# Kernel tuning notes

Measured on AMD Instinct MI355X. Metric: run time of the kernel, lower is better.

## Reference

```python
import jax, jax.numpy as jnp
import numpy as np
from itertools import permutations

NUM_LAYERS = 3
K = 5  # fixed node degree -> every Hungarian sub-problem is 5x5
# one-hot permutation tensor: P1H[p, r, c] = 1 iff permutation p assigns row r -> col c
PERMS = np.array(list(permutations(range(K))), dtype=np.int32)          # [120, K]
P1H = (PERMS[:, :, None] == np.arange(K)[None, None, :]).astype(np.float32)  # [120, K, K]


def _mlp(x, W1, b1, W2, b2):
    # 2-layer MLP with ReLU (repo's MLP(in, hid, out, 2))
    return jax.nn.relu(x @ W1 + b1) @ W2 + b2


def _sinkhorn(src, itera):
    s = jax.nn.softmax(src, axis=1)  # row-max subtraction is built in
    for i in range(itera):
        s = s / jnp.sum(s, axis=i % 2, keepdims=True)
    return jnp.nan_to_num(s)


def _masked_softmax(src):
    s1 = jnp.nan_to_num(jax.nn.softmax(src, axis=1))
    s2 = jnp.nan_to_num(jax.nn.softmax(src, axis=0))
    return (s1 + s2) * 0.5


def setup_inputs() -> dict:
    key = jax.random.key(0)
    ks = jax.random.split(key, 12)
    n1 = n2 = 1024
    hid = 64
    adj1 = jax.random.randint(ks[0], (n1, K), 0, n1)
    adj2 = jax.random.randint(ks[1], (n2, K), 0, n2)
    # adjacency matrices consistent with the neighbor lists
    G1 = jnp.zeros((n1, n1), jnp.float32).at[jnp.arange(n1)[:, None], adj1].set(1.0)
    G2 = jnp.zeros((n2, n2), jnp.float32).at[jnp.arange(n2)[:, None], adj2].set(1.0)
    s = 0.1
    return {
        'G1': G1, 'G2': G2, 'adj1': adj1, 'adj2': adj2,
        'ro_W1': jax.random.normal(ks[2], (NUM_LAYERS, 1, hid), jnp.float32) * s,
        'ro_b1': jax.random.normal(ks[3], (NUM_LAYERS, hid), jnp.float32) * s,
        'ro_W2': jax.random.normal(ks[4], (NUM_LAYERS, hid, 1), jnp.float32) * s,
        'ro_b2': jax.random.normal(ks[5], (NUM_LAYERS, 1), jnp.float32) * s,
        'fin_W1': jax.random.normal(ks[6], (1, hid), jnp.float32) * s,
        'fin_b1': jax.random.normal(ks[7], (hid,), jnp.float32) * s,
        'fin_W2': jax.random.normal(ks[8], (hid, 1), jnp.float32) * s,
        'fin_b2': jax.random.normal(ks[9], (1,), jnp.float32) * s,
    }


def reference(G1, G2, adj1, adj2, ro_W1, ro_b1, ro_W2, ro_b2, fin_W1, fin_b1, fin_W2, fin_b2):
    n1 = G1.shape[0]
    n2 = G2.shape[0]
    d1 = jnp.sum(G1, axis=1)
    d2 = jnp.sum(G2, axis=1)
    ttheta = jnp.mean(d1)
    # S[i, j, 0] = -|d1[i] - d2[j]|
    S = -jnp.abs(d1[:, None] - d2[None, :])[..., None]  # [n1, n2, 1]
    p1h = jnp.asarray(P1H)
    for li in range(NUM_LAYERS):
        Wn = _sinkhorn(_mlp(S / ttheta, ro_W1[li], ro_b1[li], ro_W2[li], ro_b2[li]).squeeze(-1), 5)
        W = jnp.log(Wn * (n1 * 1.5))
        W = jnp.where(jnp.isneginf(W), jnp.float32(-1e12), W)
        W = jnp.where(jnp.isposinf(W), jnp.float32(1e12), W)
        Wd = jax.lax.stop_gradient(W)  # matches W.detach().numpy()
        # small[a, b, r, c] = Wd[adj1[a, r], adj2[b, c]]  -> [n1, n2, K, K]
        small = jnp.transpose(Wd[adj1][:, :, adj2], (0, 2, 1, 3))
        # exact linear_sum_assignment(-small): maximize sum over the K! permutations
        scores = jnp.einsum('abrc,prc->abp', small, p1h)  # [n1, n2, 120]
        X1 = jnp.max(scores, axis=-1)                      # [n1, n2]
        S = X1[..., None]
    out = _masked_softmax(_mlp(S, fin_W1, fin_b1, fin_W2, fin_b2).squeeze(-1))
    return out
```

## Files before the change

### kernel.cpp

```cpp
#include <hip/hip_runtime.h>
#include <math.h>

#define N 1024
#define NB 256
#define KD 5
#define SL 8
#define MAGIC 0x13572468
#define FSTRIDE 32
#define FREGION (NB * FSTRIDE + FSTRIDE)


__device__ __forceinline__ float load_sc(const float* p){
  return __hip_atomic_load(p, __ATOMIC_RELAXED, __HIP_MEMORY_SCOPE_AGENT);
}
__device__ __forceinline__ void store_sc(float* p, float v){
  __hip_atomic_store(p, v, __ATOMIC_RELAXED, __HIP_MEMORY_SCOPE_AGENT);
}
__device__ __forceinline__ int load_sci(const int* p){
  return __hip_atomic_load(p, __ATOMIC_RELAXED, __HIP_MEMORY_SCOPE_AGENT);
}
__device__ __forceinline__ void store_sci(int* p, int v){
  __hip_atomic_store(p, v, __ATOMIC_RELAXED, __HIP_MEMORY_SCOPE_AGENT);
}

__device__ __forceinline__ void gbarS(int* flg){
  __builtin_amdgcn_s_waitcnt(0);
  __syncthreads();
  const int t = threadIdx.x, B = blockIdx.x;
  int* go = flg + NB * FSTRIDE;
  if (B == 0){
    if (t > 0 && t < NB){
      while (load_sci(&flg[t * FSTRIDE]) != MAGIC) __builtin_amdgcn_s_sleep(2);
    }
    __syncthreads();
    if (t == 0) store_sci(go, MAGIC);
  } else {
    if (t == 0){
      store_sci(&flg[B * FSTRIDE], MAGIC);
      while (load_sci(go) != MAGIC) __builtin_amdgcn_s_sleep(2);
    }
    __syncthreads();
  }
}

__device__ __forceinline__ float wred_sum(float v){
#pragma unroll
  for (int off = 32; off > 0; off >>= 1) v += __shfl_down(v, off);
  return v;
}
__device__ __forceinline__ void bsum4(float v[4], float* s64){
  float w0 = wred_sum(v[0]), w1 = wred_sum(v[1]), w2 = wred_sum(v[2]), w3 = wred_sum(v[3]);
  __syncthreads();
  int wv = threadIdx.x >> 6;
  if ((threadIdx.x & 63) == 0){ s64[wv*4] = w0; s64[wv*4+1] = w1; s64[wv*4+2] = w2; s64[wv*4+3] = w3; }
  __syncthreads();
  float r0 = 0.f, r1 = 0.f, r2 = 0.f, r3 = 0.f;
#pragma unroll
  for (int i = 0; i < 16; ++i){ r0 += s64[i*4]; r1 += s64[i*4+1]; r2 += s64[i*4+2]; r3 += s64[i*4+3]; }
  v[0] = r0; v[1] = r1; v[2] = r2; v[3] = r3;
}

__device__ __forceinline__ int distinct5(const int* v){
  int c = 0;
#pragma unroll
  for (int r = 0; r < KD; ++r){
    bool dup = false;
#pragma unroll
    for (int s = 0; s < r; ++s) dup = dup || (v[s] == v[r]);
    c += dup ? 0 : 1;
  }
  return c;
}

__global__ __launch_bounds__(1024) void
kX1_0(const int* __restrict__ adj1, const int* __restrict__ adj2,
      const float* __restrict__ l0W1, const float* __restrict__ l0B1,
      const float* __restrict__ l0W2, const float* __restrict__ l0B2,
      const float* __restrict__ w1g, const float* __restrict__ b1g,
      const float* __restrict__ w2g, const float* __restrict__ b2g,
      float* __restrict__ tnx, float* __restrict__ CnB, float* __restrict__ ttp)
{
  __shared__ int sd1[N], sd2[N];
  __shared__ int h1[8], h2[8];
  __shared__ float sY[25], slR[5], slC[5], stt[1];
  __shared__ float s64[64];
  __shared__ float ux[64], udA[64], udB[64], xs_s[64], dA_s[64], dB_s[64];
  __shared__ float A_tab[65], B_tab[65], sA0B0[2];
  const int t = threadIdx.x, B = blockIdx.x;

  if (t < 8){ h1[t] = 0; h2[t] = 0; }
  __syncthreads();

  int a2[KD];
#pragma unroll
  for (int c = 0; c < KD; ++c) a2[c] = adj2[t * KD + c];
  int d2v = distinct5(a2);
  sd2[t] = d2v;
  atomicAdd(&h2[d2v - 1], 1);
  {
    int v1[KD];
#pragma unroll
    for (int r = 0; r < KD; ++r) v1[r] = adj1[t * KD + r];
    int d1v = distinct5(v1);
    sd1[t] = d1v;
    atomicAdd(&h1[d1v - 1], 1);
  }
  __syncthreads();

  if (t < 64){
    float cnt1[5], cnt2[5];
#pragma unroll
    for (int g = 0; g < 5; ++g){ cnt1[g] = (float)h1[g]; cnt2[g] = (float)h2[g]; }
    float tt = 0.f;
#pragma unroll
    for (int g = 0; g < 5; ++g) tt += (float)(g + 1) * cnt1[g];
    tt *= (1.0f / 1024.0f);
    float tab[5];
#pragma unroll 1
    for (int i = 0; i < 5; ++i){
      float x = -(float)i / tt;
      float acc = l0B2[0];
      for (int k = 0; k < 64; ++k){
        float hh = fmaxf(fmaf(x, l0W1[k], l0B1[k]), 0.f);
        acc = fmaf(hh, l0W2[k], acc);
      }
      tab[i] = acc;
    }
    float Ee[5][5];
#pragma unroll
    for (int g = 0; g < 5; ++g)
#pragma unroll
      for (int h = 0; h < 5; ++h) Ee[g][h] = expf(tab[abs(g - h)]);
    float q0[5], C1c[5], q1[5], C2c[5], q2[5], C3c[5];
#pragma unroll
    for (int g = 0; g < 5; ++g){
      float s = 0.f;
#pragma unroll
      for (int h = 0; h < 5; ++h) s += cnt2[h] * Ee[g][h];
      q0[g] = s;
    }
#pragma unroll
    for (int h = 0; h < 5; ++h){
      float s = 0.f;
#pragma unroll
      for (int g = 0; g < 5; ++g) s += cnt1[g] * Ee[g][h] / q0[g];
      C1c[h] = s;
    }
#pragma unroll
    for (int g = 0; g < 5; ++g){
      float s = 0.f;
#pragma unroll
      for (int h = 0; h < 5; ++h) s += cnt2[h] * Ee[g][h] / C1c[h];
      q1[g] = s;
    }
#pragma unroll
    for (int h = 0; h < 5; ++h){
      float s = 0.f;
#pragma unroll
      for (int g = 0; g < 5; ++g) s += cnt1[g] * Ee[g][h] / q1[g];
      C2c[h] = s;
    }
#pragma unroll
    for (int g = 0; g < 5; ++g){
      float s = 0.f;
#pragma unroll
      for (int h = 0; h < 5; ++h) s += cnt2[h] * Ee[g][h] / C2c[h];
      q2[g] = s;
    }
#pragma unroll
    for (int h = 0; h < 5; ++h){
      float s = 0.f;
#pragma unroll
      for (int g = 0; g < 5; ++g) s += cnt1[g] * Ee[g][h] / q2[g];
      C3c[h] = s;
    }
    if (t == 0){
#pragma unroll
      for (int g = 0; g < 5; ++g){
#pragma unroll
        for (int h = 0; h < 5; ++h) sY[g * 5 + h] = tab[abs(g - h)];
        slR[g] = -logf(q2[g]);
        slC[g] = logf(C3c[g]);
      }
      stt[0] = tt;
      if (B == 0) ttp[0] = tt;
    }
  } else if (t < 128){
    int l = t - 64;
    float w1 = w1g[l], bb = b1g[l], w2v = w2g[l];
    float xk, sdA, sdB, a0t = 0.f, b0t = 0.f;
    if (w1 != 0.f){
      xk = -bb / w1;
      float dA = w1 * w2v, dB = bb * w2v;
      if (w1 > 0.f){ sdA = dA;  sdB = dB; }
      else         { sdA = -dA; sdB = -dB; a0t = dA; b0t = dB; }
    } else {
      xk = 3.0e38f; sdA = 0.f; sdB = 0.f;
      b0t = fmaxf(bb, 0.f) * w2v;
    }
    ux[l] = xk; udA[l] = sdA; udB[l] = sdB;
    float A0 = wred_sum(a0t);
    float B0 = wred_sum(b0t);
    if (l == 0){ sA0B0[0] = A0; sA0B0[1] = B0 + b2g[0]; }
  }
  __syncthreads();
  if (t < 64){
    float xk = ux[t]; int rank = 0;
    for (int j = 0; j < 64; ++j){
      float xj = ux[j];
      rank += (xj < xk || (xj == xk && j < t)) ? 1 : 0;
    }
    xs_s[rank] = ux[t]; dA_s[rank] = udA[t]; dB_s[rank] = udB[t];
  }
  __syncthreads();
  if (t < 65){
    float sa = sA0B0[0], sb = sA0B0[1];
    for (int r = 0; r < t; ++r){ sa += dA_s[r]; sb += dB_s[r]; }
    A_tab[t] = sa; B_tab[t] = sb;
  }
  __syncthreads();

  const float tt = stt[0];
  const float L1536 = logf(1536.0f);
  int hc[KD];
  float Bvl = 0.f;
#pragma unroll
  for (int c = 0; c < KD; ++c){ hc[c] = sd2[a2[c]] - 1; Bvl -= slC[hc[c]]; }

  float y[4];
#pragma unroll 1
  for (int rr = 0; rr < 4; ++rr){
    float Arow = 5.0f * L1536;
    float f[32];
    f[0] = 0.f;
#pragma unroll
    for (int r = 0; r < KD; ++r){
      int gr = sd1[adj1[(4 * B + rr) * KD + r]] - 1;
      Arow += slR[gr];
      float tr[KD];
#pragma unroll
      for (int c = 0; c < KD; ++c) tr[c] = sY[gr * 5 + hc[c]];
#pragma unroll
      for (int m = 1; m < 32; ++m){
        if (__popc(m) == r + 1){
          float best = -3.0e38f;
#pragma unroll
          for (int c = 0; c < KD; ++c)
            if (m & (1 << c)) best = fmaxf(best, f[m ^ (1 << c)] + tr[c]);
          f[m] = best;
        }
      }
    }
    float X1v = Arow + Bvl + f[31];
    float x = X1v / tt;
    int seg = 0;
#pragma unroll
    for (int s = 64; s; s >>= 1)
      if (seg + s <= 64 && xs_s[seg + s - 1] <= x) seg += s;
    y[rr] = fmaf(A_tab[seg], x, B_tab[seg]);
  }
  float e4[4], q4[4];
#pragma unroll
  for (int r = 0; r < 4; ++r){
    tnx[(size_t)(4 * B + r) * N + t] = y[r];
    e4[r] = expf(y[r]);
    q4[r] = e4[r];
  }
  bsum4(q4, s64);
  float cp = 0.f;
#pragma unroll
  for (int r = 0; r < 4; ++r) cp += e4[r] / q4[r];
  atomicAdd(&CnB[(size_t)(B & (SL - 1)) * N + t], cp);
}

__global__ __launch_bounds__(1024) void
kLayer(const float* __restrict__ tm, const int* __restrict__ adj1, const int* __restrict__ adj2,
       const float* __restrict__ ttp,
       const float* __restrict__ C1B, float* __restrict__ C2B, float* __restrict__ C3B,
       float* __restrict__ CnB, float* __restrict__ Rg,
       const float* __restrict__ w1g, const float* __restrict__ b1g,
       const float* __restrict__ w2g, const float* __restrict__ b2g,
       int isFinal, float* __restrict__ tnx,
       int* __restrict__ bar1, int* __restrict__ bar2, int* __restrict__ bar3)
{
  __shared__ __align__(16) float rows20[20][N];
  __shared__ float lc[N];
  __shared__ float s64[64];
  __shared__ float sAv[4];
  __shared__ float ux[64], udA[64], udB[64], xs_s[64], dA_s[64], dB_s[64];
  __shared__ float A_tab[65], B_tab[65], sA0B0[2];
  const int t = threadIdx.x, B = blockIdx.x;

  const float tt = ttp[0];
  int a2[KD];
#pragma unroll
  for (int c = 0; c < KD; ++c) a2[c] = adj2[t * KD + c];

  {
    int w = t >> 6, lane = t & 63;
    int seg = w & 3;
    int rbase = w >> 2;
#pragma unroll
    for (int k = 0; k < 5; ++k){
      int r2 = rbase + 4 * k;
      int src = adj1[(4 * B + (r2 / 5)) * KD + (r2 % 5)];
      const float* g = tm + (size_t)src * N + seg * 256 + lane * 4;
      __builtin_amdgcn_global_load_lds(
          (const __attribute__((address_space(1))) unsigned int*)g,
          (__attribute__((address_space(3))) unsigned int*)&rows20[r2][seg * 256],
          16, 0, 0);
    }
  }
  float E[4], q4[4];
#pragma unroll
  for (int r = 0; r < 4; ++r) E[r] = expf(tm[(size_t)(4 * B + r) * N + t]);

  if (t < 64){
    float w1 = w1g[t], bb = b1g[t], w2 = w2g[t];
    float xk, sdA, sdB, a0t = 0.f, b0t = 0.f;
    if (w1 != 0.f){
      xk = -bb / w1;
      float dA = w1 * w2, dB = bb * w2;
      if (w1 > 0.f){ sdA = dA;  sdB = dB; }
      else         { sdA = -dA; sdB = -dB; a0t = dA; b0t = dB; }
    } else {
      xk = 3.0e38f; sdA = 0.f; sdB = 0.f;
      b0t = fmaxf(bb, 0.f) * w2;
    }
    ux[t] = xk; udA[t] = sdA; udB[t] = sdB;
    float A0 = wred_sum(a0t);
    float B0 = wred_sum(b0t);
    if (t == 0){ sA0B0[0] = A0; sA0B0[1] = B0 + b2g[0]; }
  }
  __syncthreads();
  if (t < 64){
    float xk = ux[t]; int rank = 0;
    for (int j = 0; j < 64; ++j){
      float xj = ux[j];
      rank += (xj < xk || (xj == xk && j < t)) ? 1 : 0;
    }
    xs_s[rank] = ux[t]; dA_s[rank] = udA[t]; dB_s[rank] = udB[t];
  }
  __syncthreads();
  if (t < 65){
    float sa = sA0B0[0], sb = sA0B0[1];
    for (int r = 0; r < t; ++r){ sa += dA_s[r]; sb += dB_s[r]; }
    A_tab[t] = sa; B_tab[t] = sb;
  }

  {
    float C = 0.f;
#pragma unroll
    for (int k = 0; k < SL; ++k) C += C1B[(size_t)k * N + t];
    float iC = 1.0f / C;
#pragma unroll
    for (int r = 0; r < 4; ++r) q4[r] = E[r] * iC;
    bsum4(q4, s64);
    float cp = 0.f;
#pragma unroll
    for (int r = 0; r < 4; ++r) cp += E[r] / q4[r];
    atomicAdd(&C2B[(size_t)(B & (SL - 1)) * N + t], cp);
  }

  gbarS(bar1);
  {
    float C = 0.f;
#pragma unroll
    for (int k = 0; k < SL; ++k) C += load_sc(&C2B[(size_t)k * N + t]);
    float iC = 1.0f / C;
#pragma unroll
    for (int r = 0; r < 4; ++r) q4[r] = E[r] * iC;
    bsum4(q4, s64);
    float cp = 0.f;
#pragma unroll
    for (int r = 0; r < 4; ++r) cp += E[r] / q4[r];
    if (t < 4) store_sc(&Rg[4 * B + t], 1.0f / q4[t]);
    atomicAdd(&C3B[(size_t)(B & (SL - 1)) * N + t], cp);
  }

  gbarS(bar2);
  {
    float C = 0.f;
#pragma unroll
    for (int k = 0; k < SL; ++k) C += load_sc(&C3B[(size_t)k * N + t]);
    lc[t] = logf(C);
  }
  if (t >= 64 && t < 68){
    int a = 4 * B + (t - 64);
    float s = 5.0f * logf(1536.0f);
#pragma unroll
    for (int r = 0; r < KD; ++r) s += logf(load_sc(&Rg[adj1[a * KD + r]]));
    sAv[t - 64] = s;
  }
  __syncthreads();

  float Bvl = 0.f;
#pragma unroll
  for (int c = 0; c < KD; ++c) Bvl -= lc[a2[c]];

  float y[4];
#pragma unroll 1
  for (int rr = 0; rr < 4; ++rr){
    float f[32];
    f[0] = 0.f;
#pragma unroll
    for (int r = 0; r < KD; ++r){
      float tr[KD];
#pragma unroll
      for (int c = 0; c < KD; ++c) tr[c] = rows20[rr * 5 + r][a2[c]];
#pragma unroll
      for (int m = 1; m < 32; ++m){
        if (__popc(m) == r + 1){
          float best = -3.0e38f;
#pragma unroll
          for (int c = 0; c < KD; ++c)
            if (m & (1 << c)) best = fmaxf(best, f[m ^ (1 << c)] + tr[c]);
          f[m] = best;
        }
      }
    }
    float X1v = sAv[rr] + Bvl + f[31];
    float x = isFinal ? X1v : (X1v / tt);
    int seg = 0;
#pragma unroll
    for (int s = 64; s; s >>= 1)
      if (seg + s <= 64 && xs_s[seg + s - 1] <= x) seg += s;
    y[rr] = fmaf(A_tab[seg], x, B_tab[seg]);
  }

  float e4[4];
#pragma unroll
  for (int r = 0; r < 4; ++r){ e4[r] = expf(y[r]); q4[r] = e4[r]; }
  bsum4(q4, s64);

  if (!isFinal){
    float cp = 0.f;
#pragma unroll
    for (int r = 0; r < 4; ++r){
      tnx[(size_t)(4 * B + r) * N + t] = y[r];
      cp += e4[r] / q4[r];
    }
    atomicAdd(&CnB[(size_t)(B & (SL - 1)) * N + t], cp);
  } else {
    float cp = 0.f;
#pragma unroll
    for (int r = 0; r < 4; ++r) cp += e4[r];
    atomicAdd(&CnB[(size_t)(B & (SL - 1)) * N + t], cp);
    gbarS(bar3);
    float CF = 0.f;
#pragma unroll
    for (int k = 0; k < SL; ++k) CF += load_sc(&CnB[(size_t)k * N + t]);
    float iCF = 1.0f / CF;
#pragma unroll
    for (int r = 0; r < 4; ++r){
      float v = 0.5f * e4[r] * (1.0f / q4[r] + iCF);
      tnx[(size_t)(4 * B + r) * N + t] = v;
    }
  }
}

extern "C" void kernel_launch(void* const* d_in, const int* in_sizes, int n_in,
                              void* d_out, int out_size, void* d_ws, size_t ws_size,
                              hipStream_t stream){
  (void)in_sizes; (void)n_in; (void)out_size; (void)ws_size;
  const int*   adj1 = (const int*)d_in[2];
  const int*   adj2 = (const int*)d_in[3];
  const float* roW1 = (const float*)d_in[4];
  const float* roB1 = (const float*)d_in[5];
  const float* roW2 = (const float*)d_in[6];
  const float* roB2 = (const float*)d_in[7];
  const float* fW1  = (const float*)d_in[8];
  const float* fB1  = (const float*)d_in[9];
  const float* fW2  = (const float*)d_in[10];
  const float* fB2  = (const float*)d_in[11];
  float* out = (float*)d_out;

  float* wsA = (float*)d_ws;
  float* Pp  = wsA + (size_t)N * N;
  float* Rg  = Pp + (size_t)7 * SL * N;
  float* ttp = Rg + N;
  int*   flg = (int*)(ttp + 8);

  kX1_0<<<NB, 1024, 0, stream>>>(adj1, adj2, roW1, roB1, roW2, roB2,
                                 roW1 + 64, roB1 + 64, roW2 + 64, roB2 + 1,
                                 wsA, Pp, ttp);
  kLayer<<<NB, 1024, 0, stream>>>(wsA, adj1, adj2, ttp,
                                  Pp + (size_t)0 * SL * N, Pp + (size_t)1 * SL * N,
                                  Pp + (size_t)2 * SL * N, Pp + (size_t)3 * SL * N, Rg,
                                  roW1 + 128, roB1 + 128, roW2 + 128, roB2 + 2,
                                  0, out,
                                  flg + 0 * FREGION, flg + 1 * FREGION, flg + 2 * FREGION);
  kLayer<<<NB, 1024, 0, stream>>>(out, adj1, adj2, ttp,
                                  Pp + (size_t)3 * SL * N, Pp + (size_t)4 * SL * N,
                                  Pp + (size_t)5 * SL * N, Pp + (size_t)6 * SL * N, Rg,
                                  fW1, fB1, fW2, fB2,
                                  1, out,
                                  flg + 2 * FREGION, flg + 3 * FREGION, flg + 4 * FREGION);
}
```

Measured before the change: 161.9 us.

## Collapse layer-1 into 126x126 neighbor-type table computed per block, drop one kernel

Nodes are classified by the sorted multiset of their neighbors' distinct-degree classes, which gives 126 types. Layer 1's sinkhorn and assignment are then computed exactly on a 126x126 type table inside the first kernel, with 8-lane reductions replacing the grid-wide passes. This removes the whole middle kLayer launch and its three grid barriers over the full 1024x1024 matrix. In exchange, every block redundantly computes about 16k 5x5 DPs plus the sinkhorn, and the kernel uses much more shared memory (a 63KB table).

```diff
diff --git a/kernel.cpp b/kernel.cpp
--- a/kernel.cpp
+++ b/kernel.cpp
@@ -5,6 +5,7 @@
 #define NB 256
 #define KD 5
 #define SL 8
+#define NT 126
 #define MAGIC 0x13572468
 #define FSTRIDE 32
 #define FREGION (NB * FSTRIDE + FSTRIDE)
@@ -71,41 +72,109 @@
   }
   return c;
 }
+__device__ __forceinline__ void sort5(int* s){
+#pragma unroll
+  for (int i = 0; i < 4; ++i)
+#pragma unroll
+    for (int j = 0; j < 4 - i; ++j){
+      int a = s[j], b = s[j+1];
+      s[j] = min(a, b); s[j+1] = max(a, b);
+    }
+}
+
+#define DP5(ACCESS, OUT) {                                        \
+  float f[32]; f[0] = 0.f;                                        \
+  _Pragma("unroll")                                               \
+  for (int r = 0; r < KD; ++r){                                   \
+    float tr[KD];                                                 \
+    _Pragma("unroll")                                             \
+    for (int c = 0; c < KD; ++c) tr[c] = (ACCESS);                \
+    _Pragma("unroll")                                             \
+    for (int m = 1; m < 32; ++m){                                 \
+      if (__popc(m) == r + 1){                                    \
+        float best = -3.0e38f;                                    \
+        _Pragma("unroll")                                         \
+        for (int c = 0; c < KD; ++c)                              \
+          if (m & (1 << c)) best = fmaxf(best, f[m ^ (1 << c)] + tr[c]); \
+        f[m] = best;                                              \
+      }                                                           \
+    }                                                             \
+  }                                                               \
+  OUT = f[31];                                                    \
+}
 
 __global__ __launch_bounds__(1024) void
-kX1_0(const int* __restrict__ adj1, const int* __restrict__ adj2,
-      const float* __restrict__ l0W1, const float* __restrict__ l0B1,
-      const float* __restrict__ l0W2, const float* __restrict__ l0B2,
-      const float* __restrict__ w1g, const float* __restrict__ b1g,
-      const float* __restrict__ w2g, const float* __restrict__ b2g,
-      float* __restrict__ tnx, float* __restrict__ CnB, float* __restrict__ ttp)
+kAll0(const int* __restrict__ adj1, const int* __restrict__ adj2,
+      const float* __restrict__ roW1, const float* __restrict__ roB1,
+      const float* __restrict__ roW2, const float* __restrict__ roB2,
+      float* __restrict__ t2out, float* __restrict__ C1B)
 {
-  __shared__ int sd1[N], sd2[N];
+  __shared__ float tY1[NT * NT];
+  __shared__ unsigned short map5[3125];
+  __shared__ unsigned char t2c[NT][5];
+  __shared__ unsigned char sg1[N], sg2[N];
+  __shared__ unsigned short st1[N], st2[N];
   __shared__ int h1[8], h2[8];
-  __shared__ float sY[25], slR[5], slC[5], stt[1];
+  __shared__ int cnt1T[NT], cnt2T[NT];
+  __shared__ float A1[NT], B1[NT];
+  __shared__ float slR1[NT], slC1[NT];
+  __shared__ float vq[NT], vC[NT], vqi[NT], vCi[NT];
+  __shared__ float sY0[25], slR0[5], slC0[5], stt2[2];
   __shared__ float s64[64];
-  __shared__ float ux[64], udA[64], udB[64], xs_s[64], dA_s[64], dB_s[64];
-  __shared__ float A_tab[65], B_tab[65], sA0B0[2];
+  __shared__ float sAv[4];
+  __shared__ float ux[128], udA[128], udB[128];
+  __shared__ float xs1[64], dA1[64], dB1[64], xs2[64], dA2[64], dB2[64];
+  __shared__ float At1[65], Bt1[65], At2[65], Bt2[65];
+  __shared__ float sA0B0[4];
+
   const int t = threadIdx.x, B = blockIdx.x;
+  const float L1536 = logf(1536.0f);
 
   if (t < 8){ h1[t] = 0; h2[t] = 0; }
-  __syncthreads();
-
-  int a2[KD];
+  if (t < NT){ cnt1T[t] = 0; cnt2T[t] = 0; }
+  if (t == 1023){
+    int idx = 0;
+    for (int d0 = 0; d0 < 5; ++d0)
+     for (int d1 = d0; d1 < 5; ++d1)
+      for (int d2 = d1; d2 < 5; ++d2)
+       for (int d3 = d2; d3 < 5; ++d3)
+        for (int d4 = d3; d4 < 5; ++d4){
+          int key = d0 + 5 * (d1 + 5 * (d2 + 5 * (d3 + 5 * d4)));
+          map5[key] = (unsigned short)idx;
+          t2c[idx][0] = d0; t2c[idx][1] = d1; t2c[idx][2] = d2;
+          t2c[idx][3] = d3; t2c[idx][4] = d4;
+          ++idx;
+        }
+  }
+  int a2[KD], a1v[KD];
 #pragma unroll
   for (int c = 0; c < KD; ++c) a2[c] = adj2[t * KD + c];
-  int d2v = distinct5(a2);
-  sd2[t] = d2v;
-  atomicAdd(&h2[d2v - 1], 1);
+#pragma unroll
+  for (int r = 0; r < KD; ++r) a1v[r] = adj1[t * KD + r];
+  int g2 = distinct5(a2) - 1;
+  int g1 = distinct5(a1v) - 1;
+  sg2[t] = (unsigned char)g2; atomicAdd(&h2[g2], 1);
+  sg1[t] = (unsigned char)g1; atomicAdd(&h1[g1], 1);
+  __syncthreads();
+
   {
-    int v1[KD];
-#pragma unroll
-    for (int r = 0; r < KD; ++r) v1[r] = adj1[t * KD + r];
-    int d1v = distinct5(v1);
-    sd1[t] = d1v;
-    atomicAdd(&h1[d1v - 1], 1);
-  }
-  __syncthreads();
+    int c5[KD];
+#pragma unroll
+    for (int r = 0; r < KD; ++r) c5[r] = sg1[a1v[r]];
+    sort5(c5);
+    int key = c5[0] + 5 * (c5[1] + 5 * (c5[2] + 5 * (c5[3] + 5 * c5[4])));
+    int ty = map5[key];
+    st1[t] = (unsigned short)ty; atomicAdd(&cnt1T[ty], 1);
+  }
+  {
+    int c5[KD];
+#pragma unroll
+    for (int c = 0; c < KD; ++c) c5[c] = sg2[a2[c]];
+    sort5(c5);
+    int key = c5[0] + 5 * (c5[1] + 5 * (c5[2] + 5 * (c5[3] + 5 * c5[4])));
+    int ty = map5[key];
+    st2[t] = (unsigned short)ty; atomicAdd(&cnt2T[ty], 1);
+  }
 
   if (t < 64){
     float cnt1[5], cnt2[5];
@@ -119,10 +188,10 @@
 #pragma unroll 1
     for (int i = 0; i < 5; ++i){
       float x = -(float)i / tt;
-      float acc = l0B2[0];
+      float acc = roB2[0];
       for (int k = 0; k < 64; ++k){
-        float hh = fmaxf(fmaf(x, l0W1[k], l0B1[k]), 0.f);
-        acc = fmaf(hh, l0W2[k], acc);
+        float hh = fmaxf(fmaf(x, roW1[k], roB1[k]), 0.f);
+        acc = fmaf(hh, roW2[k], acc);
       }
       tab[i] = acc;
     }
@@ -178,15 +247,19 @@
 #pragma unroll
       for (int g = 0; g < 5; ++g){
 #pragma unroll
-        for (int h = 0; h < 5; ++h) sY[g * 5 + h] = tab[abs(g - h)];
-        slR[g] = -logf(q2[g]);
-        slC[g] = logf(C3c[g]);
+        for (int h = 0; h < 5; ++h) sY0[g * 5 + h] = tab[abs(g - h)];
+        slR0[g] = -logf(q2[g]);
+        slC0[g] = logf(C3c[g]);
       }
-      stt[0] = tt;
-      if (B == 0) ttp[0] = tt;
-    }
-  } else if (t < 128){
-    int l = t - 64;
+      stt2[0] = tt;
+    }
+  } else if (t < 192){
+    int set = (t < 128) ? 0 : 1;
+    int l = t - 64 - set * 64;
+    const float* w1g = roW1 + (set + 1) * 64;
+    const float* b1g = roB1 + (set + 1) * 64;
+    const float* w2g = roW2 + (set + 1) * 64;
+    const float* b2g = roB2 + (set + 1);
     float w1 = w1g[l], bb = b1g[l], w2v = w2g[l];
     float xk, sdA, sdB, a0t = 0.f, b0t = 0.f;
     if (w1 != 0.f){
@@ -198,90 +271,166 @@
       xk = 3.0e38f; sdA = 0.f; sdB = 0.f;
       b0t = fmaxf(bb, 0.f) * w2v;
     }
-    ux[l] = xk; udA[l] = sdA; udB[l] = sdB;
+    ux[set * 64 + l] = xk; udA[set * 64 + l] = sdA; udB[set * 64 + l] = sdB;
     float A0 = wred_sum(a0t);
     float B0 = wred_sum(b0t);
-    if (l == 0){ sA0B0[0] = A0; sA0B0[1] = B0 + b2g[0]; }
-  }
-  __syncthreads();
+    if (l == 0){ sA0B0[2 * set] = A0; sA0B0[2 * set + 1] = B0 + b2g[0]; }
+  }
+  __syncthreads();
+
   if (t < 64){
     float xk = ux[t]; int rank = 0;
     for (int j = 0; j < 64; ++j){
       float xj = ux[j];
       rank += (xj < xk || (xj == xk && j < t)) ? 1 : 0;
     }
-    xs_s[rank] = ux[t]; dA_s[rank] = udA[t]; dB_s[rank] = udB[t];
+    xs1[rank] = ux[t]; dA1[rank] = udA[t]; dB1[rank] = udB[t];
+  } else if (t < 128){
+    int l = t - 64;
+    float xk = ux[64 + l]; int rank = 0;
+    for (int j = 0; j < 64; ++j){
+      float xj = ux[64 + j];
+      rank += (xj < xk || (xj == xk && j < l)) ? 1 : 0;
+    }
+    xs2[rank] = ux[64 + l]; dA2[rank] = udA[64 + l]; dB2[rank] = udB[64 + l];
+  } else if (t >= 256 && t < 256 + NT){
+    int ty = t - 256;
+    float sa = 5.0f * L1536, sb = 0.f;
+#pragma unroll
+    for (int i = 0; i < KD; ++i){
+      int cl = t2c[ty][i];
+      sa += slR0[cl];
+      sb -= slC0[cl];
+    }
+    A1[ty] = sa; B1[ty] = sb;
   }
   __syncthreads();
   if (t < 65){
     float sa = sA0B0[0], sb = sA0B0[1];
-    for (int r = 0; r < t; ++r){ sa += dA_s[r]; sb += dB_s[r]; }
-    A_tab[t] = sa; B_tab[t] = sb;
-  }
-  __syncthreads();
-
-  const float tt = stt[0];
-  const float L1536 = logf(1536.0f);
-  int hc[KD];
-  float Bvl = 0.f;
-#pragma unroll
-  for (int c = 0; c < KD; ++c){ hc[c] = sd2[a2[c]] - 1; Bvl -= slC[hc[c]]; }
+    for (int r = 0; r < t; ++r){ sa += dA1[r]; sb += dB1[r]; }
+    At1[t] = sa; Bt1[t] = sb;
+  } else if (t >= 128 && t < 193){
+    int l = t - 128;
+    float sa = sA0B0[2], sb = sA0B0[3];
+    for (int r = 0; r < l; ++r){ sa += dA2[r]; sb += dB2[r]; }
+    At2[l] = sa; Bt2[l] = sb;
+  }
+  __syncthreads();
+
+  const float tt = stt2[0];
+#pragma unroll 1
+  for (int e = t; e < NT * NT; e += 1024){
+    int tau = e / NT, ups = e - tau * NT;
+    const unsigned char* G = t2c[tau];
+    const unsigned char* H = t2c[ups];
+    float D;
+    DP5(sY0[(int)G[r] * 5 + (int)H[c]], D);
+    float x = (A1[tau] + B1[ups] + D) / tt;
+    int seg = 0;
+#pragma unroll
+    for (int s = 64; s; s >>= 1)
+      if (seg + s <= 64 && xs1[seg + s - 1] <= x) seg += s;
+    tY1[e] = fmaf(At1[seg], x, Bt1[seg]);
+  }
+  __syncthreads();
+
+  {
+    int g = t >> 3, j = t & 7;
+    if (g < NT){
+      float acc = 0.f;
+      for (int u = j; u < NT; u += 8) acc += (float)cnt2T[u] * expf(tY1[g * NT + u]);
+      acc += __shfl_down(acc, 4, 8); acc += __shfl_down(acc, 2, 8); acc += __shfl_down(acc, 1, 8);
+      if (j == 0){ vq[g] = acc; vqi[g] = 1.0f / acc; }
+    }
+    __syncthreads();
+    if (g < NT){
+      float acc = 0.f;
+      for (int u = j; u < NT; u += 8) acc += (float)cnt1T[u] * expf(tY1[u * NT + g]) * vqi[u];
+      acc += __shfl_down(acc, 4, 8); acc += __shfl_down(acc, 2, 8); acc += __shfl_down(acc, 1, 8);
+      if (j == 0){ vC[g] = acc; vCi[g] = 1.0f / acc; }
+    }
+    __syncthreads();
+    if (g < NT){
+      float acc = 0.f;
+      for (int u = j; u < NT; u += 8) acc += (float)cnt2T[u] * expf(tY1[g * NT + u]) * vCi[u];
+      acc += __shfl_down(acc, 4, 8); acc += __shfl_down(acc, 2, 8); acc += __shfl_down(acc, 1, 8);
+      if (j == 0){ vq[g] = acc; vqi[g] = 1.0f / acc; }
+    }
+    __syncthreads();
+    if (g < NT){
+      float acc = 0.f;
+      for (int u = j; u < NT; u += 8) acc += (float)cnt1T[u] * expf(tY1[u * NT + g]) * vqi[u];
+      acc += __shfl_down(acc, 4, 8); acc += __shfl_down(acc, 2, 8); acc += __shfl_down(acc, 1, 8);
+      if (j == 0){ vC[g] = acc; vCi[g] = 1.0f / acc; }
+    }
+    __syncthreads();
+    if (g < NT){
+      float acc = 0.f;
+      for (int u = j; u < NT; u += 8) acc += (float)cnt2T[u] * expf(tY1[g * NT + u]) * vCi[u];
+      acc += __shfl_down(acc, 4, 8); acc += __shfl_down(acc, 2, 8); acc += __shfl_down(acc, 1, 8);
+      if (j == 0){ vq[g] = acc; vqi[g] = 1.0f / acc; }
+    }
+    __syncthreads();
+    if (g < NT){
+      float acc = 0.f;
+      for (int u = j; u < NT; u += 8) acc += (float)cnt1T[u] * expf(tY1[u * NT + g]) * vqi[u];
+      acc += __shfl_down(acc, 4, 8); acc += __shfl_down(acc, 2, 8); acc += __shfl_down(acc, 1, 8);
+      if (j == 0) vC[g] = acc;
+    }
+    __syncthreads();
+  }
+  if (t < NT){ slR1[t] = -logf(vq[t]); slC1[t] = logf(vC[t]); }
+  __syncthreads();
+
+  if (t < 4){
+    int a = 4 * B + t;
+    float s = 5.0f * L1536;
+#pragma unroll
+    for (int r = 0; r < KD; ++r) s += slR1[st1[adj1[a * KD + r]]];
+    sAv[t] = s;
+  }
+  int stc[KD];
+  float Bv2 = 0.f;
+#pragma unroll
+  for (int c = 0; c < KD; ++c){ stc[c] = st2[a2[c]]; Bv2 -= slC1[stc[c]]; }
+  __syncthreads();
 
   float y[4];
 #pragma unroll 1
   for (int rr = 0; rr < 4; ++rr){
-    float Arow = 5.0f * L1536;
-    float f[32];
-    f[0] = 0.f;
-#pragma unroll
-    for (int r = 0; r < KD; ++r){
-      int gr = sd1[adj1[(4 * B + rr) * KD + r]] - 1;
-      Arow += slR[gr];
-      float tr[KD];
-#pragma unroll
-      for (int c = 0; c < KD; ++c) tr[c] = sY[gr * 5 + hc[c]];
-#pragma unroll
-      for (int m = 1; m < 32; ++m){
-        if (__popc(m) == r + 1){
-          float best = -3.0e38f;
-#pragma unroll
-          for (int c = 0; c < KD; ++c)
-            if (m & (1 << c)) best = fmaxf(best, f[m ^ (1 << c)] + tr[c]);
-          f[m] = best;
-        }
-      }
-    }
-    float X1v = Arow + Bvl + f[31];
-    float x = X1v / tt;
+    int str_[KD];
+#pragma unroll
+    for (int r = 0; r < KD; ++r) str_[r] = st1[adj1[(4 * B + rr) * KD + r]];
+    float D;
+    DP5(tY1[str_[r] * NT + stc[c]], D);
+    float x = (sAv[rr] + Bv2 + D) / tt;
     int seg = 0;
 #pragma unroll
     for (int s = 64; s; s >>= 1)
-      if (seg + s <= 64 && xs_s[seg + s - 1] <= x) seg += s;
-    y[rr] = fmaf(A_tab[seg], x, B_tab[seg]);
+      if (seg + s <= 64 && xs2[seg + s - 1] <= x) seg += s;
+    y[rr] = fmaf(At2[seg], x, Bt2[seg]);
   }
   float e4[4], q4[4];
 #pragma unroll
-  for (int r = 0; r < 4; ++r){
-    tnx[(size_t)(4 * B + r) * N + t] = y[r];
-    e4[r] = expf(y[r]);
-    q4[r] = e4[r];
-  }
+  for (int r = 0; r < 4; ++r){ e4[r] = expf(y[r]); q4[r] = e4[r]; }
   bsum4(q4, s64);
   float cp = 0.f;
 #pragma unroll
-  for (int r = 0; r < 4; ++r) cp += e4[r] / q4[r];
-  atomicAdd(&CnB[(size_t)(B & (SL - 1)) * N + t], cp);
+  for (int r = 0; r < 4; ++r){
+    t2out[(size_t)(4 * B + r) * N + t] = y[r];
+    cp += e4[r] / q4[r];
+  }
+  atomicAdd(&C1B[(size_t)(B & (SL - 1)) * N + t], cp);
 }
 
 __global__ __launch_bounds__(1024) void
-kLayer(const float* __restrict__ tm, const int* __restrict__ adj1, const int* __restrict__ adj2,
-       const float* __restrict__ ttp,
-       const float* __restrict__ C1B, float* __restrict__ C2B, float* __restrict__ C3B,
-       float* __restrict__ CnB, float* __restrict__ Rg,
-       const float* __restrict__ w1g, const float* __restrict__ b1g,
-       const float* __restrict__ w2g, const float* __restrict__ b2g,
-       int isFinal, float* __restrict__ tnx,
-       int* __restrict__ bar1, int* __restrict__ bar2, int* __restrict__ bar3)
+kLayerF(const float* __restrict__ tm, const int* __restrict__ adj1, const int* __restrict__ adj2,
+        const float* __restrict__ C1B, float* __restrict__ C2B, float* __restrict__ C3B,
+        float* __restrict__ CFB, float* __restrict__ Rg,
+        const float* __restrict__ w1g, const float* __restrict__ b1g,
+        const float* __restrict__ w2g, const float* __restrict__ b2g,
+        float* __restrict__ outp,
+        int* __restrict__ bar1, int* __restrict__ bar2, int* __restrict__ bar3)
 {
   __shared__ __align__(16) float rows20[20][N];
   __shared__ float lc[N];
@@ -291,7 +440,6 @@
   __shared__ float A_tab[65], B_tab[65], sA0B0[2];
   const int t = threadIdx.x, B = blockIdx.x;
 
-  const float tt = ttp[0];
   int a2[KD];
 #pragma unroll
   for (int c = 0; c < KD; ++c) a2[c] = adj2[t * KD + c];
@@ -401,26 +549,9 @@
   float y[4];
 #pragma unroll 1
   for (int rr = 0; rr < 4; ++rr){
-    float f[32];
-    f[0] = 0.f;
-#pragma unroll
-    for (int r = 0; r < KD; ++r){
-      float tr[KD];
-#pragma unroll
-      for (int c = 0; c < KD; ++c) tr[c] = rows20[rr * 5 + r][a2[c]];
-#pragma unroll
-      for (int m = 1; m < 32; ++m){
-        if (__popc(m) == r + 1){
-          float best = -3.0e38f;
-#pragma unroll
-          for (int c = 0; c < KD; ++c)
-            if (m & (1 << c)) best = fmaxf(best, f[m ^ (1 << c)] + tr[c]);
-          f[m] = best;
-        }
-      }
-    }
-    float X1v = sAv[rr] + Bvl + f[31];
-    float x = isFinal ? X1v : (X1v / tt);
+    float D;
+    DP5(rows20[rr * 5 + r][a2[c]], D);
+    float x = sAv[rr] + Bvl + D;
     int seg = 0;
 #pragma unroll
     for (int s = 64; s; s >>= 1)
@@ -433,29 +564,20 @@
   for (int r = 0; r < 4; ++r){ e4[r] = expf(y[r]); q4[r] = e4[r]; }
   bsum4(q4, s64);
 
-  if (!isFinal){
-    float cp = 0.f;
-#pragma unroll
-    for (int r = 0; r < 4; ++r){
-      tnx[(size_t)(4 * B + r) * N + t] = y[r];
-      cp += e4[r] / q4[r];
-    }
-    atomicAdd(&CnB[(size_t)(B & (SL - 1)) * N + t], cp);
-  } else {
-    float cp = 0.f;
-#pragma unroll
-    for (int r = 0; r < 4; ++r) cp += e4[r];
-    atomicAdd(&CnB[(size_t)(B & (SL - 1)) * N + t], cp);
-    gbarS(bar3);
-    float CF = 0.f;
-#pragma unroll
-    for (int k = 0; k < SL; ++k) CF += load_sc(&CnB[(size_t)k * N + t]);
-    float iCF = 1.0f / CF;
-#pragma unroll
-    for (int r = 0; r < 4; ++r){
-      float v = 0.5f * e4[r] * (1.0f / q4[r] + iCF);
-      tnx[(size_t)(4 * B + r) * N + t] = v;
-    }
+  float cp = 0.f;
+#pragma unroll
+  for (int r = 0; r < 4; ++r) cp += e4[r];
+  atomicAdd(&CFB[(size_t)(B & (SL - 1)) * N + t], cp);
+
+  gbarS(bar3);
+  float CF = 0.f;
+#pragma unroll
+  for (int k = 0; k < SL; ++k) CF += load_sc(&CFB[(size_t)k * N + t]);
+  float iCF = 1.0f / CF;
+#pragma unroll
+  for (int r = 0; r < 4; ++r){
+    float v = 0.5f * e4[r] * (1.0f / q4[r] + iCF);
+    outp[(size_t)(4 * B + r) * N + t] = v;
   }
 }
 
@@ -475,25 +597,14 @@
   const float* fB2  = (const float*)d_in[11];
   float* out = (float*)d_out;
 
-  float* wsA = (float*)d_ws;
-  float* Pp  = wsA + (size_t)N * N;
-  float* Rg  = Pp + (size_t)7 * SL * N;
-  float* ttp = Rg + N;
-  int*   flg = (int*)(ttp + 8);
-
-  kX1_0<<<NB, 1024, 0, stream>>>(adj1, adj2, roW1, roB1, roW2, roB2,
-                                 roW1 + 64, roB1 + 64, roW2 + 64, roB2 + 1,
-                                 wsA, Pp, ttp);
-  kLayer<<<NB, 1024, 0, stream>>>(wsA, adj1, adj2, ttp,
-                                  Pp + (size_t)0 * SL * N, Pp + (size_t)1 * SL * N,
-                                  Pp + (size_t)2 * SL * N, Pp + (size_t)3 * SL * N, Rg,
-                                  roW1 + 128, roB1 + 128, roW2 + 128, roB2 + 2,
-                                  0, out,
-                                  flg + 0 * FREGION, flg + 1 * FREGION, flg + 2 * FREGION);
-  kLayer<<<NB, 1024, 0, stream>>>(out, adj1, adj2, ttp,
-                                  Pp + (size_t)3 * SL * N, Pp + (size_t)4 * SL * N,
-                                  Pp + (size_t)5 * SL * N, Pp + (size_t)6 * SL * N, Rg,
-                                  fW1, fB1, fW2, fB2,
-                                  1, out,
-                                  flg + 2 * FREGION, flg + 3 * FREGION, flg + 4 * FREGION);
-}
+  float* Pp = (float*)d_ws;
+  float* Rg = Pp + (size_t)4 * SL * N;
+  int*  flg = (int*)(Rg + N);
+
+  kAll0<<<NB, 1024, 0, stream>>>(adj1, adj2, roW1, roB1, roW2, roB2, out, Pp);
+  kLayerF<<<NB, 1024, 0, stream>>>(out, adj1, adj2,
+                                   Pp + (size_t)0 * SL * N, Pp + (size_t)1 * SL * N,
+                                   Pp + (size_t)2 * SL * N, Pp + (size_t)3 * SL * N, Rg,
+                                   fW1, fB1, fW2, fB2, out,
+                                   flg + 0 * FREGION, flg + 1 * FREGION, flg + 2 * FREGION);
+}
```

Result: slower. 177.4 us (+9.6%).
